# Kernel tuning notes

Hardware: AMD Instinct MI355X
Metric: run time of the kernel (lower is better)

## Reference

```python
import jax, jax.numpy as jnp
import numpy as np
from jax import lax

NUM_ITERATIONS = 200  # matches num_iterations=200 in the torch module
MAX_DET = 100         # fixed max number of boxes per image (jit-static)


def setup_inputs() -> dict:
    key = jax.random.key(0)
    B, C, H, W = 32, 1, 512, 512
    # uint8-range image; after /255 and >0.5 threshold ~half the pixels are foreground
    image = jax.random.randint(key, (B, C, H, W), 0, 256).astype(jnp.float32)
    return {"image": image}


def _batch_mask_to_boxes(image, num_iterations, max_det):
    x = image / 255.0                      # the module's image.div(255.0)
    mask = x[:, 0] > 0.5                   # [B,H,W] foreground mask
    B, H, W = mask.shape
    HW = H * W
    m_i = mask.astype(jnp.int32)

    # unique positive label per foreground pixel, 0 = background
    labels0 = jnp.arange(1, HW + 1, dtype=jnp.int32).reshape(1, H, W) * m_i

    # connected components via iterative 3x3 max-pool label propagation
    def step(lab, _):
        lab = lax.reduce_window(lab, jnp.int32(0), lax.max,
                                (1, 3, 3), (1, 1, 1), "SAME") * m_i
        return lab, None

    labels, _ = lax.scan(step, labels0, None, length=num_iterations)

    # per-(image, label) bounding boxes via segment reductions
    seg = labels.reshape(B, HW) + (jnp.arange(B, dtype=jnp.int32) * (HW + 1))[:, None]
    seg = seg.reshape(-1)                                             # [B*HW]
    rows = jnp.broadcast_to(jnp.arange(H, dtype=jnp.float32)[None, :, None], (B, H, W)).reshape(-1)
    cols = jnp.broadcast_to(jnp.arange(W, dtype=jnp.float32)[None, None, :], (B, H, W)).reshape(-1)
    nseg = B * (HW + 1)
    ymin = jax.ops.segment_min(rows, seg, num_segments=nseg)
    ymax = jax.ops.segment_max(rows, seg, num_segments=nseg)
    xmin = jax.ops.segment_min(cols, seg, num_segments=nseg)
    xmax = jax.ops.segment_max(cols, seg, num_segments=nseg)
    counts = jax.ops.segment_sum(jnp.ones_like(rows), seg, num_segments=nseg)

    counts = counts.reshape(B, HW + 1).at[:, 0].set(0.0)  # drop background
    boxes_all = jnp.stack([xmin, ymin, xmax, ymax], axis=-1).reshape(B, HW + 1, 4)

    # keep the max_det largest components per image (fixed output shape)
    top_counts, top_idx = lax.top_k(counts, max_det)                  # [B,max_det]
    boxes = jnp.take_along_axis(boxes_all, top_idx[:, :, None], axis=1)  # [B,max_det,4]
    valid = (top_counts > 0.0)[:, :, None]
    return jnp.where(valid, boxes, 0.0)


def reference(image):
    return _batch_mask_to_boxes(image, NUM_ITERATIONS, MAX_DET)
```

## Files before the change

kernel.cpp:

```cpp
#include <hip/hip_runtime.h>
#include <cstdint>

#define IW 512
#define IH 512
#define HW 262144
#define NIMG 32
#define MAXD 100
#define TH 64
#define HALO 8
#define CX 112
#define CY 48
#define NPASS 25
#define NTX 5
#define NTY 11
#define GH 32768
#define SLOTS 2048

#define OFF_LABB  33554688ull
#define OFF_SMALL 25165824ull

__device__ __forceinline__ int imax3(int a, int b, int c) {
    int m = a > b ? a : b;
    return m > c ? m : c;
}

__global__ __launch_bounds__(256) void init_labels(const float4* __restrict__ img,
                                                   int4* __restrict__ lab) {
    const size_t n = (size_t)NIMG * HW / 4;
    const size_t stride = (size_t)gridDim.x * 256;
    for (size_t i = (size_t)blockIdx.x * 256 + threadIdx.x; i < n; i += stride) {
        float4 f = img[i];
        int p = (int)((i * 4) & (HW - 1));
        int4 o;
        o.x = (f.x > 127.5f) ? p + 1 : 0;
        o.y = (f.y > 127.5f) ? p + 2 : 0;
        o.z = (f.z > 127.5f) ? p + 3 : 0;
        o.w = (f.w > 127.5f) ? p + 4 : 0;
        lab[i] = o;
    }
}

__global__ __launch_bounds__(64) void prop_pass(const int* __restrict__ in,
                                                int* __restrict__ out) {
    const int img = blockIdx.z;
    const int x0 = blockIdx.x * CX - HALO;
    const int y0 = blockIdx.y * CY - HALO;
    const int lane = threadIdx.x;
    const int xe = x0 + 2 * lane;
    const bool colok = (xe >= 0) && (xe < IW);
    const int2* __restrict__ ip2 = (const int2*)(in + (size_t)img * HW);
    int2* __restrict__ op2 = (int2*)(out + (size_t)img * HW);

    int a[TH], b[TH];
#pragma unroll
    for (int i = 0; i < TH; ++i) {
        int gy = y0 + i;
        int2 ld = make_int2(0, 0);
        if (colok && gy >= 0 && gy < IH) ld = ip2[gy * (IW / 2) + (xe >> 1)];
        a[i] = ld.x; b[i] = ld.y;
    }

#pragma unroll 1
    for (int it = 0; it < HALO; ++it) {
        int la0 = __shfl_up(b[0], 1, 64);
        int ra0 = __shfl_down(a[0], 1, 64);
        int haP = 0, hbP = 0;
        int haC = imax3(la0, a[0], b[0]);
        int hbC = imax3(a[0], b[0], ra0);
#pragma unroll
        for (int i = 0; i < TH; ++i) {
            int haN = 0, hbN = 0;
            if (i < TH - 1) {
                int l = __shfl_up(b[i + 1], 1, 64);
                int r = __shfl_down(a[i + 1], 1, 64);
                haN = imax3(l, a[i + 1], b[i + 1]);
                hbN = imax3(a[i + 1], b[i + 1], r);
            }
            int na = imax3(haP, haC, haN);
            int nb = imax3(hbP, hbC, hbN);
            a[i] = (a[i] == 0) ? 0 : na;
            b[i] = (b[i] == 0) ? 0 : nb;
            haP = haC; haC = haN; hbP = hbC; hbC = hbN;
        }
    }

    if (lane >= 4 && lane < 60 && colok) {
#pragma unroll
        for (int i = HALO; i < TH - HALO; ++i) {
            int gy = y0 + i;
            if (gy < IH) op2[gy * (IW / 2) + (xe >> 1)] = make_int2(a[i], b[i]);
        }
    }
}

__device__ __forceinline__ unsigned gfind(unsigned* __restrict__ gk, unsigned key) {
    unsigned h = (key * 2654435761u) >> 17;
    for (unsigned pr = 0; pr < GH; ++pr) {
        unsigned idx = (h + pr) & (GH - 1);
        unsigned k = gk[idx];
        if (k == key) return idx;
        if (k == 0u) {
            unsigned old = atomicCAS(&gk[idx], 0u, key);
            if (old == 0u || old == key) return idx;
        }
    }
    return h;
}

__global__ __launch_bounds__(256) void stat_pass(const int* __restrict__ lab,
                                                 unsigned* __restrict__ gk,
                                                 unsigned* __restrict__ gcnt,
                                                 unsigned* __restrict__ gx0,
                                                 unsigned* __restrict__ gx1,
                                                 unsigned* __restrict__ gy0,
                                                 unsigned* __restrict__ gy1) {
    __shared__ unsigned hk[SLOTS], hc[SLOTS];
    __shared__ unsigned sx0[SLOTS], sx1[SLOTS], sy0[SLOTS], sy1[SLOTS];
    const int img = blockIdx.y;
    const int rb = blockIdx.x * 16;
    const int t = threadIdx.x;
    for (int i = t; i < SLOTS; i += 256) {
        hk[i] = 0; hc[i] = 0;
        sx0[i] = 0xFFFFFFFFu; sy0[i] = 0xFFFFFFFFu; sx1[i] = 0; sy1[i] = 0;
    }
    __syncthreads();
    unsigned* gki = gk + (size_t)img * GH;
    unsigned* gci = gcnt + (size_t)img * GH;
    unsigned* gx0i = gx0 + (size_t)img * GH;
    unsigned* gx1i = gx1 + (size_t)img * GH;
    unsigned* gy0i = gy0 + (size_t)img * GH;
    unsigned* gy1i = gy1 + (size_t)img * GH;

    const int4* lp = (const int4*)(lab + (size_t)img * HW + rb * IW);
    for (int i = t; i < 16 * IW / 4; i += 256) {
        int4 v = lp[i];
        unsigned y = (unsigned)(rb + (i >> 7));
        unsigned xb = (unsigned)((i & 127) << 2);
        int larr[4] = {v.x, v.y, v.z, v.w};
#pragma unroll
        for (int e = 0; e < 4; ++e) {
            unsigned l = (unsigned)larr[e];
            if (!l) continue;
            unsigned x = xb + (unsigned)e;
            unsigned h = (l * 2654435761u) >> 21;
            int idx = -1;
            for (int pr = 0; pr < 32; ++pr) {
                unsigned j = (h + pr) & (SLOTS - 1);
                unsigned k = hk[j];
                if (k == l) { idx = (int)j; break; }
                if (k == 0u) {
                    unsigned old = atomicCAS(&hk[j], 0u, l);
                    if (old == 0u || old == l) { idx = (int)j; break; }
                }
            }
            if (idx >= 0) {
                atomicAdd(&hc[idx], 1u);
                atomicMin(&sx0[idx], x); atomicMax(&sx1[idx], x);
                atomicMin(&sy0[idx], y); atomicMax(&sy1[idx], y);
            } else {
                unsigned g = gfind(gki, l);
                atomicAdd(&gci[g], 1u);
                atomicMin(&gx0i[g], x); atomicMax(&gx1i[g], x);
                atomicMin(&gy0i[g], y); atomicMax(&gy1i[g], y);
            }
        }
    }
    __syncthreads();
    for (int i = t; i < SLOTS; i += 256) {
        unsigned k = hk[i];
        if (!k) continue;
        unsigned g = gfind(gki, k);
        atomicAdd(&gci[g], hc[i]);
        atomicMin(&gx0i[g], sx0[i]); atomicMax(&gx1i[g], sx1[i]);
        atomicMin(&gy0i[g], sy0[i]); atomicMax(&gy1i[g], sy1[i]);
    }
}

__global__ __launch_bounds__(1024) void topk(const unsigned* __restrict__ gk,
                                             const unsigned* __restrict__ gcnt,
                                             unsigned* __restrict__ rank_count,
                                             unsigned* __restrict__ rank_slot) {
    const int img = blockIdx.x;
    const int t = threadIdx.x;
    const unsigned* gki = gk + (size_t)img * GH;
    const unsigned* gci = gcnt + (size_t)img * GH;
    unsigned long long karg[32];
#pragma unroll
    for (int j = 0; j < 32; ++j) {
        int slot = j * 1024 + t;
        unsigned lb = gki[slot];
        unsigned long long key = 0;
        if (lb) {
            unsigned c = gci[slot];
            key = ((((unsigned long long)c << 19) | (unsigned)(HW - lb)) << 15)
                  | (unsigned)slot;
        }
        karg[j] = key;
    }
    unsigned live = 0xFFFFFFFFu;
    __shared__ unsigned long long wred[16];
    __shared__ unsigned long long winner;
    __shared__ unsigned s_cnt[MAXD], s_slot[MAXD];
    const int lane = t & 63, wid = t >> 6;
    for (int r = 0; r < MAXD; ++r) {
        unsigned long long m = 0;
#pragma unroll
        for (int j = 0; j < 32; ++j) {
            unsigned long long cand = ((live >> j) & 1u) ? karg[j] : 0ull;
            if (cand > m) m = cand;
        }
        for (int s = 1; s < 64; s <<= 1) {
            unsigned long long o = (unsigned long long)__shfl_xor((long long)m, s, 64);
            if (o > m) m = o;
        }
        if (lane == 0) wred[wid] = m;
        __syncthreads();
        if (wid == 0) {
            unsigned long long w = (lane < 16) ? wred[lane] : 0ull;
            for (int s = 1; s < 16; s <<= 1) {
                unsigned long long o = (unsigned long long)__shfl_xor((long long)w, s, 64);
                if (o > w) w = o;
            }
            if (lane == 0) winner = w;
        }
        __syncthreads();
        unsigned long long w = winner;
        int slot = (int)(w & 32767ull);
        if (t == (slot & 1023)) live &= ~(1u << (slot >> 10));
        if (t == 0) { s_cnt[r] = (unsigned)(w >> 34); s_slot[r] = (unsigned)(w & 32767ull); }
        __syncthreads();
    }
    if (t < MAXD) {
        rank_count[img * MAXD + t] = s_cnt[t];
        rank_slot[img * MAXD + t] = s_slot[t];
    }
}

__global__ __launch_bounds__(256) void final_out(const unsigned* __restrict__ rank_count,
                                                 const unsigned* __restrict__ rank_slot,
                                                 const unsigned* __restrict__ gx0,
                                                 const unsigned* __restrict__ gx1,
                                                 const unsigned* __restrict__ gy0,
                                                 const unsigned* __restrict__ gy1,
                                                 float* __restrict__ out) {
    int id = blockIdx.x * 256 + threadIdx.x;
    if (id >= NIMG * MAXD) return;
    unsigned c = rank_count[id];
    float4 b = make_float4(0.f, 0.f, 0.f, 0.f);
    if (c) {
        int img = id / MAXD;
        size_t g = (size_t)img * GH + rank_slot[id];
        b = make_float4((float)gx0[g], (float)gy0[g], (float)gx1[g], (float)gy1[g]);
    }
    reinterpret_cast<float4*>(out)[id] = b;
}

extern "C" void kernel_launch(void* const* d_in, const int* in_sizes, int n_in,
                              void* d_out, int out_size, void* d_ws, size_t ws_size,
                              hipStream_t stream) {
    (void)in_sizes; (void)n_in; (void)out_size; (void)ws_size;
    const float* img = (const float*)d_in[0];
    char* ws = (char*)d_ws;

    int* labA = (int*)ws;
    int* labB = (int*)(ws + OFF_LABB);
    unsigned* gk   = (unsigned*)ws;
    unsigned* gcnt = (unsigned*)(ws + 4194304ull);
    unsigned* gx1  = (unsigned*)(ws + 8388608ull);
    unsigned* gy1  = (unsigned*)(ws + 12582912ull);
    unsigned* gx0  = (unsigned*)(ws + 16777216ull);
    unsigned* gy0  = (unsigned*)(ws + 20971520ull);
    unsigned* rank_count = (unsigned*)(ws + OFF_SMALL);
    unsigned* rank_slot  = (unsigned*)(ws + OFF_SMALL + 16384ull);
    float* out = (float*)d_out;

    init_labels<<<2048, 256, 0, stream>>>((const float4*)img, (int4*)labA);

    dim3 pg(NTX, NTY, NIMG);
    const int* pin = labA; int* pout = labB;
    for (int p = 0; p < NPASS; ++p) {
        prop_pass<<<pg, 64, 0, stream>>>(pin, pout);
        int* tmp = (int*)pin; pin = pout; pout = tmp;
    }

    hipMemsetAsync(gk, 0, 16777216ull, stream);
    hipMemsetAsync(gx0, 0xFF, 8388608ull, stream);

    stat_pass<<<dim3(32, NIMG), 256, 0, stream>>>(pin, gk, gcnt, gx0, gx1, gy0, gy1);
    topk<<<NIMG, 1024, 0, stream>>>(gk, gcnt, rank_count, rank_slot);
    final_out<<<(NIMG * MAXD + 255) / 256, 256, 0, stream>>>(rank_count, rank_slot,
                                                             gx0, gx1, gy0, gy1, out);
}
```

Baseline: 1.268 ms.

## Compact live components into LDS for top-k and retile propagation to 48-row tiles

The top-k kernel now gathers the non-empty hash slots into a shared-memory key array and keeps a per-thread cached maximum. Only the thread owning each round's winner rescans its strided slice, instead of every thread re-reducing 32 register keys each round, and it runs with 256 threads instead of 1024. Separately, the propagation tile height shrinks from 64 to 48 rows (32 core rows, 16 y-tiles), which changes the grid shape and the halo overhead. The key buffer is capped at 12288 entries, so any image with more live components silently drops keys, and a single thread's rescan is serialized every round.

```diff
diff --git a/kernel.cpp b/kernel.cpp
--- a/kernel.cpp
+++ b/kernel.cpp
@@ -6,15 +6,16 @@
 #define HW 262144
 #define NIMG 32
 #define MAXD 100
-#define TH 64
+#define TH 48
 #define HALO 8
 #define CX 112
-#define CY 48
+#define CY 32
 #define NPASS 25
 #define NTX 5
-#define NTY 11
+#define NTY 16
 #define GH 32768
 #define SLOTS 2048
+#define CAP 12288
 
 #define OFF_LABB  33554688ull
 #define OFF_SMALL 25165824ull
@@ -176,63 +177,68 @@
     }
 }
 
-__global__ __launch_bounds__(1024) void topk(const unsigned* __restrict__ gk,
-                                             const unsigned* __restrict__ gcnt,
-                                             unsigned* __restrict__ rank_count,
-                                             unsigned* __restrict__ rank_slot) {
+__global__ __launch_bounds__(256) void topk(const unsigned* __restrict__ gk,
+                                            const unsigned* __restrict__ gcnt,
+                                            unsigned* __restrict__ rank_count,
+                                            unsigned* __restrict__ rank_slot) {
+    __shared__ unsigned long long keys[CAP];
+    __shared__ unsigned long long wred[4];
     const int img = blockIdx.x;
     const int t = threadIdx.x;
+    const int lane = t & 63, wid = t >> 6;
+    for (int i = t; i < CAP; i += 256) keys[i] = 0;
+    __shared__ unsigned ncnt;
+    if (t == 0) ncnt = 0;
+    __syncthreads();
+
     const unsigned* gki = gk + (size_t)img * GH;
     const unsigned* gci = gcnt + (size_t)img * GH;
-    unsigned long long karg[32];
-#pragma unroll
-    for (int j = 0; j < 32; ++j) {
-        int slot = j * 1024 + t;
-        unsigned lb = gki[slot];
-        unsigned long long key = 0;
+    for (int i = t; i < GH; i += 256) {
+        unsigned lb = gki[i];
         if (lb) {
-            unsigned c = gci[slot];
-            key = ((((unsigned long long)c << 19) | (unsigned)(HW - lb)) << 15)
-                  | (unsigned)slot;
-        }
-        karg[j] = key;
-    }
-    unsigned live = 0xFFFFFFFFu;
-    __shared__ unsigned long long wred[16];
-    __shared__ unsigned long long winner;
-    __shared__ unsigned s_cnt[MAXD], s_slot[MAXD];
-    const int lane = t & 63, wid = t >> 6;
+            unsigned c = gci[i];
+            unsigned long long key =
+                ((((unsigned long long)c << 19) | (unsigned)(HW - lb)) << 15)
+                | (unsigned)i;
+            unsigned pos = atomicAdd(&ncnt, 1u);
+            if (pos < CAP) keys[pos] = key;
+        }
+    }
+    __syncthreads();
+
+    unsigned long long maxv = 0; int maxi = -1;
+    for (int i = t; i < CAP; i += 256) {
+        unsigned long long k = keys[i];
+        if (k > maxv) { maxv = k; maxi = i; }
+    }
+
     for (int r = 0; r < MAXD; ++r) {
-        unsigned long long m = 0;
-#pragma unroll
-        for (int j = 0; j < 32; ++j) {
-            unsigned long long cand = ((live >> j) & 1u) ? karg[j] : 0ull;
-            if (cand > m) m = cand;
-        }
+        unsigned long long m = maxv;
         for (int s = 1; s < 64; s <<= 1) {
             unsigned long long o = (unsigned long long)__shfl_xor((long long)m, s, 64);
             if (o > m) m = o;
         }
         if (lane == 0) wred[wid] = m;
         __syncthreads();
-        if (wid == 0) {
-            unsigned long long w = (lane < 16) ? wred[lane] : 0ull;
-            for (int s = 1; s < 16; s <<= 1) {
-                unsigned long long o = (unsigned long long)__shfl_xor((long long)w, s, 64);
-                if (o > w) w = o;
-            }
-            if (lane == 0) winner = w;
+        unsigned long long w = wred[0];
+        if (wred[1] > w) w = wred[1];
+        if (wred[2] > w) w = wred[2];
+        if (wred[3] > w) w = wred[3];
+        if (w != 0ull && maxv == w) {
+            keys[maxi] = 0;
+            rank_count[img * MAXD + r] = (unsigned)(w >> 34);
+            rank_slot[img * MAXD + r]  = (unsigned)(w & 32767ull);
+            maxv = 0; maxi = -1;
+            for (int i = t; i < CAP; i += 256) {
+                unsigned long long k = keys[i];
+                if (k > maxv) { maxv = k; maxi = i; }
+            }
+        }
+        if (w == 0ull && t == 0) {
+            rank_count[img * MAXD + r] = 0;
+            rank_slot[img * MAXD + r] = 0;
         }
         __syncthreads();
-        unsigned long long w = winner;
-        int slot = (int)(w & 32767ull);
-        if (t == (slot & 1023)) live &= ~(1u << (slot >> 10));
-        if (t == 0) { s_cnt[r] = (unsigned)(w >> 34); s_slot[r] = (unsigned)(w & 32767ull); }
-        __syncthreads();
-    }
-    if (t < MAXD) {
-        rank_count[img * MAXD + t] = s_cnt[t];
-        rank_slot[img * MAXD + t] = s_slot[t];
     }
 }
 
@@ -287,7 +293,7 @@
     hipMemsetAsync(gx0, 0xFF, 8388608ull, stream);
 
     stat_pass<<<dim3(32, NIMG), 256, 0, stream>>>(pin, gk, gcnt, gx0, gx1, gy0, gy1);
-    topk<<<NIMG, 1024, 0, stream>>>(gk, gcnt, rank_count, rank_slot);
+    topk<<<NIMG, 256, 0, stream>>>(gk, gcnt, rank_count, rank_slot);
     final_out<<<(NIMG * MAXD + 255) / 256, 256, 0, stream>>>(rank_count, rank_slot,
                                                              gx0, gx1, gy0, gy1, out);
 }
```

Result: slower. 1.413 ms (+11.5%).
